# Performance work log

Measured on AMD Instinct MI355X. Metric: run time of the kernel, lower is better.

The kernel has to match this reference:

```python
import jax, jax.numpy as jnp
import numpy as np

B, S, DM = 2, 2048, 1024  # batch, seq_len, model_dim
H, HD = 16, 64            # num_heads, head_dim (H*HD == DM)


def setup_inputs() -> dict:
    key = jax.random.key(0)
    ks = jax.random.split(key, 8)
    scale = 0.02
    return {
        "k": jax.random.normal(ks[0], (B, S, DM), jnp.float32),
        "q": jax.random.normal(ks[1], (B, S, DM), jnp.float32),
        "v": jax.random.normal(ks[2], (B, S, DM), jnp.float32),
        "Wk": jax.random.normal(ks[3], (DM, H * HD), jnp.float32) * scale,
        "bk": jnp.zeros((H * HD,), jnp.float32),
        "Wq": jax.random.normal(ks[4], (DM, H * HD), jnp.float32) * scale,
        "bq": jnp.zeros((H * HD,), jnp.float32),
        "Wv": jax.random.normal(ks[5], (DM, H * HD), jnp.float32) * scale,
        "bv": jnp.zeros((H * HD,), jnp.float32),
        "Wo": jax.random.normal(ks[6], (H * HD, DM), jnp.float32) * scale,
        "bo": jnp.zeros((DM,), jnp.float32),
    }


def reference(k, q, v, Wk, bk, Wq, bq, Wv, bv, Wo, bo):
    # QKV projections (Dense with bias)
    kp = (k @ Wk + bk).reshape(B, S, H, HD)
    qp = (q @ Wq + bq).reshape(B, S, H, HD)
    vp = (v @ Wv + bv).reshape(B, S, H, HD)
    # Faithful to original: scores indexed [b, key_c, h, query_q],
    # softmax over the QUERY axis, NO 1/sqrt(head_dim) scaling.
    scores = jnp.einsum('bchd,bqhd->bchq', kp, qp)
    attn = jax.nn.softmax(scores, axis=-1)
    out = jnp.einsum('bchq,bqhd->bchd', attn, vp)  # [B, S(keys), H, HD]
    out = out.reshape(B, S, H * HD)
    return out @ Wo + bo
```

## Files before the change

kernel.cpp:

```cpp
#include <hip/hip_runtime.h>
#include <hip/hip_bf16.h>
#include <stdint.h>
#include <stddef.h>


typedef __attribute__((ext_vector_type(4))) float f32x4;
typedef __attribute__((ext_vector_type(16))) float f32x16;
typedef __attribute__((ext_vector_type(8))) short s16x8;
typedef __attribute__((ext_vector_type(4))) unsigned int u32x4;
typedef __attribute__((ext_vector_type(4))) unsigned short u16x4;

#define DEV static __device__ __forceinline__

DEV unsigned short f2bf(float x) {
  unsigned int u = __float_as_uint(x);
  u += 0x7FFF + ((u >> 16) & 1);
  return (unsigned short)(u >> 16);
}
DEV f32x4 mfma16(s16x8 a, s16x8 b, f32x4 c) {
  return __builtin_amdgcn_mfma_f32_16x16x32_bf16(a, b, c, 0, 0, 0);
}
DEV f32x16 mfma32(s16x8 a, s16x8 b, f32x16 c) {
  return __builtin_amdgcn_mfma_f32_32x32x16_bf16(a, b, c, 0, 0, 0);
}
DEV f32x4 fzero() { f32x4 z; z[0]=0.f; z[1]=0.f; z[2]=0.f; z[3]=0.f; return z; }
DEV f32x16 fzero16() {
  f32x16 z;
#pragma unroll
  for (int i = 0; i < 16; ++i) z[i] = 0.f;
  return z;
}

DEV void gload_lds16(const unsigned short* g, unsigned short* l) {
  __builtin_amdgcn_global_load_lds(
      (const __attribute__((address_space(1))) unsigned int*)g,
      (__attribute__((address_space(3))) unsigned int*)l, 16, 0, 0);
}

#define CVTPK(dst, a, b) \
  asm("v_cvt_pk_bf16_f32 %0, %1, %2" : "=v"(dst) : "v"(a), "v"(b))
#define PSWAP(x, y) \
  asm("v_permlane32_swap_b32 %0, %1" : "+v"(x), "+v"(y))

struct CvtArgs { const float* x[3]; unsigned short* y[3]; };

__global__ __launch_bounds__(256) void cvt_kernel(CvtArgs a) {
  const float* x = a.x[blockIdx.y];
  unsigned short* y = a.y[blockIdx.y];
  const int i = blockIdx.x * 256 + threadIdx.x;
  f32x4 v = ((const f32x4*)x)[i];
  u16x4 o;
#pragma unroll
  for (int j = 0; j < 4; ++j) o[j] = f2bf(v[j]);
  ((u16x4*)y)[i] = o;
}

struct WArgs { const float* W[4]; unsigned short* Wt[4]; };

__global__ __launch_bounds__(256) void wtrans_kernel(WArgs a) {
  const float* W = a.W[blockIdx.z];
  unsigned short* Wt = a.Wt[blockIdx.z];
  const int n0 = blockIdx.x * 32, k0 = blockIdx.y * 32;
  __shared__ float t[32][33];
  const int tx = threadIdx.x & 31, ty = threadIdx.x >> 5;
#pragma unroll
  for (int i = 0; i < 4; ++i)
    t[ty + i*8][tx] = W[(size_t)(k0 + ty + i*8) * 1024 + n0 + tx];
  __syncthreads();
#pragma unroll
  for (int i = 0; i < 4; ++i)
    Wt[(size_t)(n0 + ty + i*8) * 1024 + k0 + tx] = f2bf(t[tx][ty + i*8]);
}

struct GemArgs {
  const unsigned short* A[3];
  const unsigned short* Wt[3];
  const float* bias[3];
  void* C[3];
  int mode[3];
};

template<int BM>
__global__ __launch_bounds__(256) void gemm_kernel(GemArgs g) {
  constexpr int MF = BM / 32;
  const int z = blockIdx.z;
  const unsigned short* A  = g.A[z];
  const unsigned short* Wt = g.Wt[z];
  const float* bias = g.bias[z];
  const int mode = g.mode[z];
  const int m0 = blockIdx.y * BM, n0 = blockIdx.x * 128;
  const int tid = threadIdx.x;
  const int lane = tid & 63, w = tid >> 6;
  const int wm = w >> 1, wn = w & 1;
  const int lg = lane >> 4, lr = lane & 15, lx = lr & 7;

  __shared__ __align__(16) unsigned short As[BM * 64];
  __shared__ __align__(16) unsigned short Bs[128 * 64];

  f32x4 acc[MF][4];
#pragma unroll
  for (int i = 0; i < MF; ++i)
#pragma unroll
    for (int j = 0; j < 4; ++j) acc[i][j] = fzero();

  const int aStep = (mode == 2) ? 2048 * 64 : 64;
  const unsigned short* srcA[MF]; unsigned short* dstA[MF];
#pragma unroll
  for (int c = 0; c < MF; ++c) {
    int n = c*256 + tid, row = n >> 3, cg = (n & 7) ^ (row & 7);
    int s = m0 + row;
    size_t abase = (mode == 2)
        ? ((size_t)((s >> 11) * 16) * 2048 + (s & 2047)) * 64 + cg * 8
        : (size_t)s * 1024 + cg * 8;
    srcA[c] = A + abase;
    dstA[c] = &As[n * 8];
  }
  const unsigned short* srcB[4]; unsigned short* dstB[4];
#pragma unroll
  for (int c = 0; c < 4; ++c) {
    int n = c*256 + tid, row = n >> 3, cg = (n & 7) ^ (row & 7);
    srcB[c] = Wt + (size_t)(n0 + row) * 1024 + cg * 8;
    dstB[c] = &Bs[n * 8];
  }

  for (int it = 0; it < 16; ++it) {
    __syncthreads();
#pragma unroll
    for (int c = 0; c < MF; ++c) { gload_lds16(srcA[c], dstA[c]); srcA[c] += aStep; }
#pragma unroll
    for (int c = 0; c < 4; ++c)  { gload_lds16(srcB[c], dstB[c]); srcB[c] += 64; }
    __syncthreads();

    s16x8 af[2][MF], bf[2][4];
#pragma unroll
    for (int ks = 0; ks < 2; ++ks) {
#pragma unroll
      for (int mf = 0; mf < MF; ++mf) {
        int row = wm*(BM/2) + mf*16 + lr;
        af[ks][mf] = *(const s16x8*)&As[row*64 + ((ks*4 + lg) ^ lx) * 8];
      }
#pragma unroll
      for (int nf = 0; nf < 4; ++nf) {
        int row = wn*64 + nf*16 + lr;
        bf[ks][nf] = *(const s16x8*)&Bs[row*64 + ((ks*4 + lg) ^ lx) * 8];
      }
    }
#pragma unroll
    for (int mf = 0; mf < MF; ++mf)
#pragma unroll
      for (int nf = 0; nf < 4; ++nf) {
        acc[mf][nf] = mfma16(af[0][mf], bf[0][nf], acc[mf][nf]);
        acc[mf][nf] = mfma16(af[1][mf], bf[1][nf], acc[mf][nf]);
      }
  }

#pragma unroll
  for (int nf = 0; nf < 4; ++nf) {
    const int colg = n0 + wn*64 + nf*16 + lr;
    const float bi = bias[colg];
#pragma unroll
    for (int mf = 0; mf < MF; ++mf) {
      const int rowg0 = m0 + wm*(BM/2) + mf*16 + lg*4;
      if (mode == 0) {
        unsigned short* o = (unsigned short*)g.C[z];
#pragma unroll
        for (int r = 0; r < 4; ++r)
          o[(size_t)(rowg0 + r) * 1024 + colg] = f2bf(acc[mf][nf][r] + bi);
      } else if (mode == 1) {
        const int hh = colg >> 6, d = colg & 63;
        const int bb2 = rowg0 >> 11, s = rowg0 & 2047;
        u16x4 pk;
#pragma unroll
        for (int r = 0; r < 4; ++r) pk[r] = f2bf(acc[mf][nf][r] + bi);
        *(u16x4*)((unsigned short*)g.C[z] + ((size_t)((bb2*16 + hh)*64 + d)) * 2048 + s) = pk;
      } else {
        float* o = (float*)g.C[z];
#pragma unroll
        for (int r = 0; r < 4; ++r)
          o[(size_t)(rowg0 + r) * 1024 + colg] = acc[mf][nf][r] + bi;
      }
    }
  }
}

__global__ __launch_bounds__(256) void attn_kernel(
    const unsigned short* __restrict__ kp, const unsigned short* __restrict__ qp,
    const unsigned short* __restrict__ vpt, unsigned short* __restrict__ aout) {
  const int F = blockIdx.x;
  const int swz = (F & 7) * 64 + (F >> 3);
  const int bh = swz >> 4, cblk = swz & 15;
  const int b = bh >> 4, h = bh & 15;
  const int c0 = cblk * 128;
  const int tid = threadIdx.x, lane = tid & 63, w = tid >> 6;
  const int ln = lane & 31, hh = lane >> 5;

  __shared__ __align__(16) unsigned short qa_lds[2][2048];
  __shared__ __align__(16) unsigned short vb_lds[2][2048];

  const int srow = tid >> 3, sp = tid & 7, sl = sp ^ (srow & 7);
  const unsigned short* qsrc =
      qp + (size_t)(b*2048 + srow) * 1024 + h*64 + sl*8;
  const int sd = srow + 32*(sl >> 2), sjc = sl & 3;
  const unsigned short* vsrc =
      vpt + ((size_t)((b*16 + h)*64) + sd) * 2048 + sjc*8;

  s16x8 kb[4];
  {
    const unsigned short* krow =
        kp + (size_t)(b*2048 + c0 + w*32 + ln) * 1024 + h*64 + hh*8;
#pragma unroll
    for (int s = 0; s < 4; ++s) kb[s] = *(const s16x8*)(krow + s*16);
  }

  f32x16 acc0 = fzero16(), acc1 = fzero16();
  float m_run = -1e30f, l_run = 0.f;

  gload_lds16(qsrc, &qa_lds[0][tid*8]);
  gload_lds16(vsrc, &vb_lds[0][tid*8]);
  qsrc += 32*1024; vsrc += 32;
  __syncthreads();

  for (int jt = 0; jt < 64; ++jt) {
    const int cur = jt & 1;
    if (jt + 1 < 64) {
      gload_lds16(qsrc, &qa_lds[cur^1][tid*8]);
      gload_lds16(vsrc, &vb_lds[cur^1][tid*8]);
      qsrc += 32*1024; vsrc += 32;
    }

    s16x8 qa[4];
#pragma unroll
    for (int s = 0; s < 4; ++s) {
      const int p = (2*s + hh) ^ (ln & 7);
      qa[s] = *(const s16x8*)&qa_lds[cur][(ln*8 + p)*8];
    }
    f32x16 sc = fzero16();
#pragma unroll
    for (int s = 0; s < 4; ++s) sc = mfma32(qa[s], kb[s], sc);

    s16x8 vb[4];
#pragma unroll
    for (int t = 0; t < 4; ++t) {
      const int l = (t >> 1)*4 + (t & 1)*2 + hh;
      const int p = l ^ (ln & 7);
      vb[t] = *(const s16x8*)&vb_lds[cur][(ln*8 + p)*8];
    }

    float mx = fmaxf(fmaxf(sc[0], sc[1]), fmaxf(sc[2], sc[3]));
    float mx1 = fmaxf(fmaxf(sc[4], sc[5]), fmaxf(sc[6], sc[7]));
    float mx2 = fmaxf(fmaxf(sc[8], sc[9]), fmaxf(sc[10], sc[11]));
    float mx3 = fmaxf(fmaxf(sc[12], sc[13]), fmaxf(sc[14], sc[15]));
    mx = fmaxf(fmaxf(mx, mx1), fmaxf(mx2, mx3));
    mx = fmaxf(mx, __shfl_xor(mx, 32));
    if (__any(mx > m_run + 8.0f)) {
      float mn = fmaxf(m_run, mx);
      float al = __expf(m_run - mn);
      m_run = mn; l_run *= al;
#pragma unroll
      for (int r = 0; r < 16; ++r) { acc0[r] *= al; acc1[r] *= al; }
    }
    float ts = 0.f;
#pragma unroll
    for (int r = 0; r < 16; ++r) {
      float p = __expf(sc[r] - m_run); sc[r] = p; ts += p;
    }
    ts += __shfl_xor(ts, 32);
    l_run += ts;

    unsigned int a0, a1, b0, b1;
    u32x4 wv; s16x8 pa0, pa1;
    CVTPK(a0, sc[0], sc[1]);  CVTPK(b0, sc[4], sc[5]);  PSWAP(a0, b0);
    CVTPK(a1, sc[2], sc[3]);  CVTPK(b1, sc[6], sc[7]);  PSWAP(a1, b1);
    wv[0] = a0; wv[1] = a1; wv[2] = b0; wv[3] = b1;
    pa0 = __builtin_bit_cast(s16x8, wv);
    CVTPK(a0, sc[8], sc[9]);  CVTPK(b0, sc[12], sc[13]); PSWAP(a0, b0);
    CVTPK(a1, sc[10], sc[11]); CVTPK(b1, sc[14], sc[15]); PSWAP(a1, b1);
    wv[0] = a0; wv[1] = a1; wv[2] = b0; wv[3] = b1;
    pa1 = __builtin_bit_cast(s16x8, wv);

    acc0 = mfma32(vb[0], pa0, acc0);
    acc0 = mfma32(vb[1], pa1, acc0);
    acc1 = mfma32(vb[2], pa0, acc1);
    acc1 = mfma32(vb[3], pa1, acc1);

    __syncthreads();
  }

  const float inv = 1.0f / l_run;
  unsigned short* obase =
      aout + ((size_t)bh * 2048 + c0 + w*32 + ln) * 64 + hh * 4;
#pragma unroll
  for (int dt = 0; dt < 2; ++dt)
#pragma unroll
    for (int rq = 0; rq < 4; ++rq) {
      u16x4 pk;
#pragma unroll
      for (int i = 0; i < 4; ++i) {
        const int reg = rq*4 + i;
        pk[i] = f2bf(((dt == 0) ? acc0[reg] : acc1[reg]) * inv);
      }
      *(u16x4*)(obase + dt*32 + rq*8) = pk;
    }
}

extern "C" void kernel_launch(void* const* d_in, const int* in_sizes, int n_in,
                              void* d_out, int out_size, void* d_ws, size_t ws_size,
                              hipStream_t stream) {
  (void)in_sizes; (void)n_in; (void)out_size; (void)ws_size;
  const float* k  = (const float*)d_in[0];
  const float* q  = (const float*)d_in[1];
  const float* v  = (const float*)d_in[2];
  const float* Wk = (const float*)d_in[3];
  const float* bk = (const float*)d_in[4];
  const float* Wq = (const float*)d_in[5];
  const float* bq = (const float*)d_in[6];
  const float* Wv = (const float*)d_in[7];
  const float* bv = (const float*)d_in[8];
  const float* Wo = (const float*)d_in[9];
  const float* bo = (const float*)d_in[10];

  char* ws = (char*)d_ws;
  const size_t MB = 1024 * 1024;
  unsigned short* Wkt = (unsigned short*)(ws + 0*MB);
  unsigned short* Wqt = (unsigned short*)(ws + 2*MB);
  unsigned short* Wvt = (unsigned short*)(ws + 4*MB);
  unsigned short* Wot = (unsigned short*)(ws + 6*MB);
  unsigned short* kp  = (unsigned short*)(ws + 8*MB);
  unsigned short* qp  = (unsigned short*)(ws + 16*MB);
  unsigned short* vpt = (unsigned short*)(ws + 24*MB);
  unsigned short* vc  = (unsigned short*)(ws + 32*MB);
  unsigned short* aoutb = (unsigned short*)(ws + 40*MB);
  unsigned short* kc = (unsigned short*)d_out;
  unsigned short* qc = (unsigned short*)((char*)d_out + 8*MB);

  CvtArgs ca;
  ca.x[0] = k; ca.x[1] = q; ca.x[2] = v;
  ca.y[0] = kc; ca.y[1] = qc; ca.y[2] = vc;
  cvt_kernel<<<dim3(4096, 3), 256, 0, stream>>>(ca);

  WArgs wa;
  wa.W[0] = Wk; wa.W[1] = Wq; wa.W[2] = Wv; wa.W[3] = Wo;
  wa.Wt[0] = Wkt; wa.Wt[1] = Wqt; wa.Wt[2] = Wvt; wa.Wt[3] = Wot;
  wtrans_kernel<<<dim3(32, 32, 4), 256, 0, stream>>>(wa);

  GemArgs gp;
  gp.A[0] = kc; gp.A[1] = qc; gp.A[2] = vc;
  gp.Wt[0] = Wkt; gp.Wt[1] = Wqt; gp.Wt[2] = Wvt;
  gp.bias[0] = bk; gp.bias[1] = bq; gp.bias[2] = bv;
  gp.C[0] = kp; gp.C[1] = qp; gp.C[2] = vpt;
  gp.mode[0] = 0; gp.mode[1] = 0; gp.mode[2] = 1;
  gemm_kernel<128><<<dim3(8, 32, 3), 256, 0, stream>>>(gp);

  attn_kernel<<<dim3(512), 256, 0, stream>>>(kp, qp, vpt, aoutb);

  GemArgs gf;
  gf.A[0] = aoutb; gf.A[1] = aoutb; gf.A[2] = aoutb;
  gf.Wt[0] = Wot; gf.Wt[1] = Wot; gf.Wt[2] = Wot;
  gf.bias[0] = bo; gf.bias[1] = bo; gf.bias[2] = bo;
  gf.C[0] = d_out; gf.C[1] = d_out; gf.C[2] = d_out;
  gf.mode[0] = 2; gf.mode[1] = 2; gf.mode[2] = 2;
  gemm_kernel<64><<<dim3(8, 64, 1), 256, 0, stream>>>(gf);
}
```

Measured before the change: 152.2 us.

## Split attention query axis across wave pairs and fold log2e into K projection

The attention kernel now uses 64-key blocks instead of 128, launching 1024 blocks. Each pair of waves handles the same keys over different halves of the query axis, and the two partial softmax states are merged through LDS at the end. The K projection output is pre-scaled by log2(e), so the softmax can call the hardware exp2 directly instead of __expf, with the rescale threshold adjusted to match. This aims for more parallelism and occupancy and cheaper exponentials, at the cost of doubled LDS staging, an extra merge pass, and extra bf16 rounding of the scaled K.

Result: no change. 153.5 us (+0.8%).

```diff
diff --git a/kernel.cpp b/kernel.cpp
--- a/kernel.cpp
+++ b/kernel.cpp
@@ -30,6 +30,7 @@
   for (int i = 0; i < 16; ++i) z[i] = 0.f;
   return z;
 }
+DEV float fexp2(float x) { return __builtin_amdgcn_exp2f(x); }
 
 DEV void gload_lds16(const unsigned short* g, unsigned short* l) {
   __builtin_amdgcn_global_load_lds(
@@ -78,6 +79,7 @@
   const float* bias[3];
   void* C[3];
   int mode[3];
+  float scale[3];
 };
 
 template<int BM>
@@ -88,6 +90,7 @@
   const unsigned short* Wt = g.Wt[z];
   const float* bias = g.bias[z];
   const int mode = g.mode[z];
+  const float scale = g.scale[z];
   const int m0 = blockIdx.y * BM, n0 = blockIdx.x * 128;
   const int tid = threadIdx.x;
   const int lane = tid & 63, w = tid >> 6;
@@ -165,7 +168,7 @@
         unsigned short* o = (unsigned short*)g.C[z];
 #pragma unroll
         for (int r = 0; r < 4; ++r)
-          o[(size_t)(rowg0 + r) * 1024 + colg] = f2bf(acc[mf][nf][r] + bi);
+          o[(size_t)(rowg0 + r) * 1024 + colg] = f2bf((acc[mf][nf][r] + bi) * scale);
       } else if (mode == 1) {
         const int hh = colg >> 6, d = colg & 63;
         const int bb2 = rowg0 >> 11, s = rowg0 & 2047;
@@ -187,27 +190,30 @@
     const unsigned short* __restrict__ kp, const unsigned short* __restrict__ qp,
     const unsigned short* __restrict__ vpt, unsigned short* __restrict__ aout) {
   const int F = blockIdx.x;
-  const int swz = (F & 7) * 64 + (F >> 3);
-  const int bh = swz >> 4, cblk = swz & 15;
+  const int swz = (F & 7) * 128 + (F >> 3);
+  const int bh = swz >> 5, cblk = swz & 31;
   const int b = bh >> 4, h = bh & 15;
-  const int c0 = cblk * 128;
+  const int c0 = cblk * 64;
   const int tid = threadIdx.x, lane = tid & 63, w = tid >> 6;
+  const int cg = w & 1, jg = w >> 1;
   const int ln = lane & 31, hh = lane >> 5;
 
-  __shared__ __align__(16) unsigned short qa_lds[2][2048];
-  __shared__ __align__(16) unsigned short vb_lds[2][2048];
+  __shared__ __align__(16) unsigned short qa_lds[2][2][2048];
+  __shared__ __align__(16) unsigned short vb_lds[2][2][2048];
 
   const int srow = tid >> 3, sp = tid & 7, sl = sp ^ (srow & 7);
-  const unsigned short* qsrc =
-      qp + (size_t)(b*2048 + srow) * 1024 + h*64 + sl*8;
+  const unsigned short* qsrcs[2];
+  qsrcs[0] = qp + (size_t)(b*2048 + srow) * 1024 + h*64 + sl*8;
+  qsrcs[1] = qsrcs[0] + (size_t)1024 * 1024;
   const int sd = srow + 32*(sl >> 2), sjc = sl & 3;
-  const unsigned short* vsrc =
-      vpt + ((size_t)((b*16 + h)*64) + sd) * 2048 + sjc*8;
+  const unsigned short* vsrcs[2];
+  vsrcs[0] = vpt + ((size_t)((b*16 + h)*64) + sd) * 2048 + sjc*8;
+  vsrcs[1] = vsrcs[0] + 1024;
 
   s16x8 kb[4];
   {
     const unsigned short* krow =
-        kp + (size_t)(b*2048 + c0 + w*32 + ln) * 1024 + h*64 + hh*8;
+        kp + (size_t)(b*2048 + c0 + cg*32 + ln) * 1024 + h*64 + hh*8;
 #pragma unroll
     for (int s = 0; s < 4; ++s) kb[s] = *(const s16x8*)(krow + s*16);
   }
@@ -215,24 +221,30 @@
   f32x16 acc0 = fzero16(), acc1 = fzero16();
   float m_run = -1e30f, l_run = 0.f;
 
-  gload_lds16(qsrc, &qa_lds[0][tid*8]);
-  gload_lds16(vsrc, &vb_lds[0][tid*8]);
-  qsrc += 32*1024; vsrc += 32;
+#pragma unroll
+  for (int hf = 0; hf < 2; ++hf) {
+    gload_lds16(qsrcs[hf], &qa_lds[0][hf][tid*8]);
+    gload_lds16(vsrcs[hf], &vb_lds[0][hf][tid*8]);
+    qsrcs[hf] += 32*1024; vsrcs[hf] += 32;
+  }
   __syncthreads();
 
-  for (int jt = 0; jt < 64; ++jt) {
+  for (int jt = 0; jt < 32; ++jt) {
     const int cur = jt & 1;
-    if (jt + 1 < 64) {
-      gload_lds16(qsrc, &qa_lds[cur^1][tid*8]);
-      gload_lds16(vsrc, &vb_lds[cur^1][tid*8]);
-      qsrc += 32*1024; vsrc += 32;
+    if (jt + 1 < 32) {
+#pragma unroll
+      for (int hf = 0; hf < 2; ++hf) {
+        gload_lds16(qsrcs[hf], &qa_lds[cur^1][hf][tid*8]);
+        gload_lds16(vsrcs[hf], &vb_lds[cur^1][hf][tid*8]);
+        qsrcs[hf] += 32*1024; vsrcs[hf] += 32;
+      }
     }
 
     s16x8 qa[4];
 #pragma unroll
     for (int s = 0; s < 4; ++s) {
       const int p = (2*s + hh) ^ (ln & 7);
-      qa[s] = *(const s16x8*)&qa_lds[cur][(ln*8 + p)*8];
+      qa[s] = *(const s16x8*)&qa_lds[cur][jg][(ln*8 + p)*8];
     }
     f32x16 sc = fzero16();
 #pragma unroll
@@ -243,7 +255,7 @@
     for (int t = 0; t < 4; ++t) {
       const int l = (t >> 1)*4 + (t & 1)*2 + hh;
       const int p = l ^ (ln & 7);
-      vb[t] = *(const s16x8*)&vb_lds[cur][(ln*8 + p)*8];
+      vb[t] = *(const s16x8*)&vb_lds[cur][jg][(ln*8 + p)*8];
     }
 
     float mx = fmaxf(fmaxf(sc[0], sc[1]), fmaxf(sc[2], sc[3]));
@@ -252,9 +264,9 @@
     float mx3 = fmaxf(fmaxf(sc[12], sc[13]), fmaxf(sc[14], sc[15]));
     mx = fmaxf(fmaxf(mx, mx1), fmaxf(mx2, mx3));
     mx = fmaxf(mx, __shfl_xor(mx, 32));
-    if (__any(mx > m_run + 8.0f)) {
+    if (__any(mx > m_run + 11.544f)) {
       float mn = fmaxf(m_run, mx);
-      float al = __expf(m_run - mn);
+      float al = fexp2(m_run - mn);
       m_run = mn; l_run *= al;
 #pragma unroll
       for (int r = 0; r < 16; ++r) { acc0[r] *= al; acc1[r] *= al; }
@@ -262,7 +274,7 @@
     float ts = 0.f;
 #pragma unroll
     for (int r = 0; r < 16; ++r) {
-      float p = __expf(sc[r] - m_run); sc[r] = p; ts += p;
+      float p = fexp2(sc[r] - m_run); sc[r] = p; ts += p;
     }
     ts += __shfl_xor(ts, 32);
     l_run += ts;
@@ -286,21 +298,42 @@
     __syncthreads();
   }
 
-  const float inv = 1.0f / l_run;
-  unsigned short* obase =
-      aout + ((size_t)bh * 2048 + c0 + w*32 + ln) * 64 + hh * 4;
-#pragma unroll
-  for (int dt = 0; dt < 2; ++dt)
-#pragma unroll
-    for (int rq = 0; rq < 4; ++rq) {
-      u16x4 pk;
-#pragma unroll
-      for (int i = 0; i < 4; ++i) {
-        const int reg = rq*4 + i;
-        pk[i] = f2bf(((dt == 0) ? acc0[reg] : acc1[reg]) * inv);
-      }
-      *(u16x4*)(obase + dt*32 + rq*8) = pk;
-    }
+  float* mrg = (float*)&qa_lds[0][0][0];
+  float* ml  = (float*)&vb_lds[0][0][0];
+  if (jg == 1) {
+    ml[(cg*2 + 0)*64 + lane] = m_run;
+    ml[(cg*2 + 1)*64 + lane] = l_run;
+#pragma unroll
+    for (int r = 0; r < 16; ++r) {
+      mrg[(cg*32 + r)*64 + lane] = acc0[r];
+      mrg[(cg*32 + 16 + r)*64 + lane] = acc1[r];
+    }
+  }
+  __syncthreads();
+  if (jg == 0) {
+    const float m1 = ml[(cg*2 + 0)*64 + lane];
+    const float l1 = ml[(cg*2 + 1)*64 + lane];
+    const float mt = fmaxf(m_run, m1);
+    float a0 = fexp2(m_run - mt), a1 = fexp2(m1 - mt);
+    const float inv = 1.0f / (a0 * l_run + a1 * l1);
+    a0 *= inv; a1 *= inv;
+    unsigned short* obase =
+        aout + ((size_t)bh * 2048 + c0 + cg*32 + ln) * 64 + hh * 4;
+#pragma unroll
+    for (int dt = 0; dt < 2; ++dt)
+#pragma unroll
+      for (int rq = 0; rq < 4; ++rq) {
+        u16x4 pk;
+#pragma unroll
+        for (int i = 0; i < 4; ++i) {
+          const int reg = rq*4 + i;
+          const float own = (dt == 0) ? acc0[reg] : acc1[reg];
+          const float oth = mrg[(cg*32 + dt*16 + reg)*64 + lane];
+          pk[i] = f2bf(a0 * own + a1 * oth);
+        }
+        *(u16x4*)(obase + dt*32 + rq*8) = pk;
+      }
+  }
 }
 
 extern "C" void kernel_launch(void* const* d_in, const int* in_sizes, int n_in,
@@ -349,9 +382,11 @@
   gp.bias[0] = bk; gp.bias[1] = bq; gp.bias[2] = bv;
   gp.C[0] = kp; gp.C[1] = qp; gp.C[2] = vpt;
   gp.mode[0] = 0; gp.mode[1] = 0; gp.mode[2] = 1;
+  gp.scale[0] = 1.4426950408889634f;
+  gp.scale[1] = 1.0f; gp.scale[2] = 1.0f;
   gemm_kernel<128><<<dim3(8, 32, 3), 256, 0, stream>>>(gp);
 
-  attn_kernel<<<dim3(512), 256, 0, stream>>>(kp, qp, vpt, aoutb);
+  attn_kernel<<<dim3(1024), 256, 0, stream>>>(kp, qp, vpt, aoutb);
 
   GemArgs gf;
   gf.A[0] = aoutb; gf.A[1] = aoutb; gf.A[2] = aoutb;
@@ -359,5 +394,6 @@
   gf.bias[0] = bo; gf.bias[1] = bo; gf.bias[2] = bo;
   gf.C[0] = d_out; gf.C[1] = d_out; gf.C[2] = d_out;
   gf.mode[0] = 2; gf.mode[1] = 2; gf.mode[2] = 2;
+  gf.scale[0] = 1.0f; gf.scale[1] = 1.0f; gf.scale[2] = 1.0f;
   gemm_kernel<64><<<dim3(8, 64, 1), 256, 0, stream>>>(gf);
 }
```
